# Performance work log

Hardware: AMD Instinct MI355X
Metric: run time of the kernel (lower is better)

Reference implementation:

```python
import jax, jax.numpy as jnp
import numpy as np

N = 50000
E = 800000
NUM_KINDS = 100
D_NODE = 64
D_EDGE = 4
D_MSG = 64
L = 3
D_IN = 2 * D_NODE + D_EDGE  # 132


def setup_inputs() -> dict:
    key = jax.random.key(0)
    ks = jax.random.split(key, 20)

    def w(k, shape, fan_in):
        bound = 1.0 / np.sqrt(fan_in)
        return jax.random.uniform(k, shape, jnp.float32, -bound, bound)

    inp = {
        "edge_index": jax.random.randint(ks[0], (2, E), 0, N),
        "node_kind_ids": jax.random.randint(ks[1], (N,), 0, NUM_KINDS),
        "edge_attr": jax.random.normal(ks[2], (E, D_EDGE), jnp.float32),
        # learned params
        "emb": jax.random.normal(ks[3], (NUM_KINDS, D_NODE), jnp.float32),
        # stacked per-layer message MLP params [L, ...]
        "msg_w1": w(ks[4], (L, D_MSG, D_IN), D_IN),
        "msg_b1": w(ks[5], (L, D_MSG), D_IN),
        "msg_w2": w(ks[6], (L, D_MSG, D_MSG), D_MSG),
        "msg_b2": w(ks[7], (L, D_MSG), D_MSG),
        # stacked per-layer GRUCell params (torch layout: [3*d_node, d_in])
        "gru_wih": w(ks[8], (L, 3 * D_NODE, D_MSG), D_NODE),
        "gru_whh": w(ks[9], (L, 3 * D_NODE, D_NODE), D_NODE),
        "gru_bih": w(ks[10], (L, 3 * D_NODE), D_NODE),
        "gru_bhh": w(ks[11], (L, 3 * D_NODE), D_NODE),
        # edge head: Linear(132,64) -> SiLU -> Linear(64,1)
        "head_w1": w(ks[12], (64, D_IN), D_IN),
        "head_b1": w(ks[13], (64,), D_IN),
        "head_w2": w(ks[14], (1, 64), 64),
        "head_b2": w(ks[15], (1,), 64),
    }
    return inp


def reference(edge_index, node_kind_ids, edge_attr, emb,
              msg_w1, msg_b1, msg_w2, msg_b2,
              gru_wih, gru_whh, gru_bih, gru_bhh,
              head_w1, head_b1, head_w2, head_b2):
    src, dst = edge_index[0], edge_index[1]
    h = emb[node_kind_ids]  # [N, d_node]
    n_nodes = h.shape[0]
    for l in range(L):
        x = jnp.concatenate([h[src], h[dst], edge_attr], axis=1)  # [E, 132]
        m = jax.nn.silu(x @ msg_w1[l].T + msg_b1[l]) @ msg_w2[l].T + msg_b2[l]  # [E, d_msg]
        agg = jax.ops.segment_sum(m, dst, num_segments=n_nodes)  # [N, d_msg]
        # torch GRUCell math
        gi = agg @ gru_wih[l].T + gru_bih[l]  # [N, 3*d_node]
        gh = h @ gru_whh[l].T + gru_bhh[l]
        ir, iz, inn = jnp.split(gi, 3, axis=1)
        hr, hz, hn = jnp.split(gh, 3, axis=1)
        r = jax.nn.sigmoid(ir + hr)
        z = jax.nn.sigmoid(iz + hz)
        n = jnp.tanh(inn + r * hn)
        h = (1.0 - z) * n + z * h
    x = jnp.concatenate([h[src], h[dst], edge_attr], axis=1)  # [E, 132]
    logits = (jax.nn.silu(x @ head_w1.T + head_b1) @ head_w2.T + head_b2)[:, 0]
    return jax.nn.sigmoid(logits)  # [E]
```

## Files before the change

kernel.cpp:

```cpp
#include <hip/hip_runtime.h>
#include <hip/hip_bf16.h>


typedef __attribute__((ext_vector_type(8))) short bf16x8;
typedef __attribute__((ext_vector_type(4))) float f32x4;
#define MFMA16(a, b, c) __builtin_amdgcn_mfma_f32_16x16x32_bf16(a, b, c, 0, 0, 0)

#define CHUNK 128
#define MSTRIDE 264
#define EBUF 8448
#define HIDB 4096

#define WRZST 264
#define WNST  136

__device__ __forceinline__ float fast_sig(float x) { return 1.f / (1.f + __expf(-x)); }
__device__ __forceinline__ float fast_tanh(float x) {
    float ax = fabsf(x);
    float t = __expf(-2.f * ax);
    return copysignf((1.f - t) / (1.f + t), x);
}
__device__ __forceinline__ ushort f2bf(float f) {
    unsigned u = __float_as_uint(f);
    unsigned r = u + 0x7FFF + ((u >> 16) & 1);
    return (ushort)(r >> 16);
}
__device__ __forceinline__ unsigned pkbf2(float a, float b) {
    unsigned r;
    asm("v_cvt_pk_bf16_f32 %0, %1, %2" : "=v"(r) : "v"(a), "v"(b));
    return r;
}

__global__ void prep_kernel(const float* __restrict__ msg_w1,
                            const float* __restrict__ msg_w2,
                            const float* __restrict__ gru_wih,
                            const float* __restrict__ gru_whh,
                            const float* __restrict__ head_w1,
                            const float* __restrict__ head_w2,
                            ushort* __restrict__ Wb1, ushort* __restrict__ Wb2,
                            ushort* __restrict__ Wh1, ushort* __restrict__ Wh2b,
                            ushort* __restrict__ Wrz, ushort* __restrict__ Wni,
                            ushort* __restrict__ Wnh) {
    int t = blockIdx.x * 256 + threadIdx.x;
    if (t < 30720) {
        int l = t / 10240, r = t % 10240, j = r / 160, k = r % 160;
        Wb1[t] = (k < 132) ? f2bf(msg_w1[l * 8448 + j * 132 + k]) : 0;
        return;
    }
    t -= 30720;
    if (t < 12288) {
        Wb2[t] = f2bf(msg_w2[t]);
        return;
    }
    t -= 12288;
    if (t < 10240) {
        int j = t / 160, k = t % 160;
        Wh1[t] = (k < 132) ? f2bf(head_w1[j * 132 + k]) : 0;
        return;
    }
    t -= 10240;
    if (t < 1024) {
        int j = t >> 6, k = t & 63;
        Wh2b[t] = (j == 0) ? f2bf(head_w2[k]) : 0;
        return;
    }
    t -= 1024;
    if (t < 49152) {
        int l = t / 16384, r = t % 16384, n = r >> 7, k = r & 127;
        float v = (k < 64) ? gru_wih[l * 12288 + n * 64 + k]
                           : gru_whh[l * 12288 + n * 64 + (k - 64)];
        Wrz[t] = f2bf(v);
        return;
    }
    t -= 49152;
    if (t < 12288) {
        int l = t / 4096, r = t % 4096, j = r >> 6, k = r & 63;
        Wni[t] = f2bf(gru_wih[l * 12288 + (128 + j) * 64 + k]);
        return;
    }
    t -= 12288;
    if (t < 12288) {
        int l = t / 4096, r = t % 4096, j = r >> 6, k = r & 63;
        Wnh[t] = f2bf(gru_whh[l * 12288 + (128 + j) * 64 + k]);
    }
}

__global__ void embed_kernel(float* __restrict__ h, ushort* __restrict__ hb,
                             const float* __restrict__ emb,
                             const int* __restrict__ kinds, int N) {
    int t = blockIdx.x * 256 + threadIdx.x;
    if (t >= N * 64) return;
    int node = t >> 6, d = t & 63;
    float v = emb[kinds[node] * 64 + d];
    h[t] = v;
    hb[t] = f2bf(v);
}

__global__ void hist_kernel(const int* __restrict__ dst, int* __restrict__ deg, int E) {
    int e = blockIdx.x * 256 + threadIdx.x;
    if (e < E) atomicAdd(&deg[dst[e]], 1);
}

__global__ void scan_kernel(const int* __restrict__ deg, int* __restrict__ cursor, int N) {
    __shared__ int sums[1024];
    int tid = threadIdx.x;
    int chunk = (N + 1023) >> 10;
    int lo = tid * chunk, hi = min(lo + chunk, N);
    int s = 0;
    for (int i = lo; i < hi; i++) s += deg[i];
    sums[tid] = s;
    __syncthreads();
    for (int off = 1; off < 1024; off <<= 1) {
        int v = (tid >= off) ? sums[tid - off] : 0;
        __syncthreads();
        sums[tid] += v;
        __syncthreads();
    }
    int run = (tid > 0) ? sums[tid - 1] : 0;
    for (int i = lo; i < hi; i++) {
        cursor[i] = run;
        run += deg[i];
    }
}

__global__ void scatter_kernel(const int* __restrict__ src, const int* __restrict__ dst,
                               const float* __restrict__ ea, int* __restrict__ cursor,
                               int* __restrict__ src_s, int* __restrict__ dst_s,
                               ushort* __restrict__ ea_sb, int E) {
    int e = blockIdx.x * 256 + threadIdx.x;
    if (e >= E) return;
    int d = dst[e];
    int p = atomicAdd(&cursor[d], 1);
    src_s[p] = src[e];
    dst_s[p] = d;
    float4 e4 = ((const float4*)ea)[e];
    ushort4 eb;
    eb.x = f2bf(e4.x); eb.y = f2bf(e4.y); eb.z = f2bf(e4.z); eb.w = f2bf(e4.w);
    ((ushort4*)ea_sb)[p] = eb;
}

__global__ __launch_bounds__(256) void edge_msg_mfma(
    const ushort* __restrict__ hb, const int* __restrict__ src_s,
    const int* __restrict__ dst_s, const ushort* __restrict__ ea_sb,
    const ushort* __restrict__ Wb1l, const ushort* __restrict__ Wb2l,
    const float* __restrict__ b1, const float* __restrict__ b2,
    float* __restrict__ agg, int E, int nchunks) {
    __shared__ char lds[4 * EBUF];
    int tid = threadIdx.x;
    int w = tid >> 6, lane = tid & 63;
    int quad = lane >> 4, nrow = lane & 15;
    char* buf = lds + w * EBUF;

    bf16x8 wf1[4][5];
    f32x4 b1q[4];
    float b2v[4];
#pragma unroll
    for (int nt = 0; nt < 4; nt++) {
        int n = nt * 16 + nrow;
#pragma unroll
        for (int ks = 0; ks < 5; ks++)
            wf1[nt][ks] = *(const bf16x8*)(Wb1l + n * 160 + ks * 32 + quad * 8);
        b1q[nt] = *(const f32x4*)(b1 + nt * 16 + quad * 4);
        b2v[nt] = b2[n];
    }

    for (int chunk = blockIdx.x; chunk < nchunks; chunk += gridDim.x) {
        int ebase = chunk * CHUNK + w * 32;
        int e0 = min(ebase + nrow, E - 1);
        int e1 = min(ebase + 16 + nrow, E - 1);
        int s0 = src_s[e0], s1 = src_s[e1];
        int d0 = dst_s[e0], d1 = dst_s[e1];

        bf16x8 x0[5], x1[5];
        {
            const ushort* p = hb + (size_t)s0 * 64 + quad * 8;
            x0[0] = *(const bf16x8*)p;
            x0[1] = *(const bf16x8*)(p + 32);
            p = hb + (size_t)d0 * 64 + quad * 8;
            x0[2] = *(const bf16x8*)p;
            x0[3] = *(const bf16x8*)(p + 32);
            p = hb + (size_t)s1 * 64 + quad * 8;
            x1[0] = *(const bf16x8*)p;
            x1[1] = *(const bf16x8*)(p + 32);
            p = hb + (size_t)d1 * 64 + quad * 8;
            x1[2] = *(const bf16x8*)p;
            x1[3] = *(const bf16x8*)(p + 32);
            bf16x8 z = {0, 0, 0, 0, 0, 0, 0, 0};
            x0[4] = z;
            x1[4] = z;
            if (quad == 0) {
                ushort4 v0 = *(const ushort4*)(ea_sb + (size_t)e0 * 4);
                ushort4 v1 = *(const ushort4*)(ea_sb + (size_t)e1 * 4);
                x0[4][0] = (short)v0.x; x0[4][1] = (short)v0.y;
                x0[4][2] = (short)v0.z; x0[4][3] = (short)v0.w;
                x1[4][0] = (short)v1.x; x1[4][1] = (short)v1.y;
                x1[4][2] = (short)v1.z; x1[4][3] = (short)v1.w;
            }
        }

        f32x4 acc[4][2];
#pragma unroll
        for (int nt = 0; nt < 4; nt++) {
            acc[nt][0] = b1q[nt];
            acc[nt][1] = b1q[nt];
        }
#pragma unroll
        for (int ks = 0; ks < 5; ks++)
#pragma unroll
            for (int nt = 0; nt < 4; nt++) {
                acc[nt][0] = MFMA16(wf1[nt][ks], x0[ks], acc[nt][0]);
                acc[nt][1] = MFMA16(wf1[nt][ks], x1[ks], acc[nt][1]);
            }

#pragma unroll
        for (int nt = 0; nt < 4; nt++)
#pragma unroll
            for (int et = 0; et < 2; et++) {
                f32x4 a = acc[nt][et];
                float v0 = a[0] * fast_sig(a[0]);
                float v1 = a[1] * fast_sig(a[1]);
                float v2 = a[2] * fast_sig(a[2]);
                float v3 = a[3] * fast_sig(a[3]);
                int er = et * 16 + nrow;
                int off = er * 128 + ((nt * 32 + quad * 8) ^ ((er & 7) << 4));
                uint2 pk;
                pk.x = pkbf2(v0, v1);
                pk.y = pkbf2(v2, v3);
                *(uint2*)(buf + off) = pk;
            }

        const ushort* wb2i = Wb2l;
        asm volatile("" : "+s"(wb2i));
        bf16x8 wf2[4][2];
#pragma unroll
        for (int nt = 0; nt < 4; nt++)
#pragma unroll
            for (int ks = 0; ks < 2; ks++)
                wf2[nt][ks] =
                    *(const bf16x8*)(wb2i + (nt * 16 + nrow) * 64 + ks * 32 + quad * 8);

        bf16x8 ha[2][2];
#pragma unroll
        for (int mt = 0; mt < 2; mt++)
#pragma unroll
            for (int ks = 0; ks < 2; ks++) {
                int er = mt * 16 + nrow;
                ha[mt][ks] = *(const bf16x8*)(
                    buf + er * 128 + ((ks * 64 + quad * 16) ^ ((er & 7) << 4)));
            }
        f32x4 acc2[2][4];
#pragma unroll
        for (int nt = 0; nt < 4; nt++) {
            f32x4 v;
            v[0] = v[1] = v[2] = v[3] = b2v[nt];
            acc2[0][nt] = v;
            acc2[1][nt] = v;
        }
#pragma unroll
        for (int ks = 0; ks < 2; ks++)
#pragma unroll
            for (int nt = 0; nt < 4; nt++) {
                acc2[0][nt] = MFMA16(ha[0][ks], wf2[nt][ks], acc2[0][nt]);
                acc2[1][nt] = MFMA16(ha[1][ks], wf2[nt][ks], acc2[1][nt]);
            }

#pragma unroll
        for (int mt = 0; mt < 2; mt++)
#pragma unroll
            for (int nt = 0; nt < 4; nt++)
#pragma unroll
                for (int rg = 0; rg < 4; rg++) {
                    int rm = mt * 16 + quad * 4 + rg;
                    *(float*)(buf + rm * MSTRIDE + (nt * 16 + nrow) * 4) =
                        acc2[mt][nt][rg];
                }

        {
            int dmy = (lane & 16) ? d1 : d0;
            int limit = min(32, E - ebase);
            int nx = __shfl_down(dmy, 1);
            bool tl = ((lane & 31) == 31) || (dmy != nx);
            unsigned long long tm = __ballot(tl);
            float run = 0.f;
#pragma unroll
            for (int i = 0; i < 32; i++) {
                if (i < limit) {
                    run += *(const float*)(buf + i * MSTRIDE + lane * 4);
                    if (((tm >> i) & 1ull) || (i + 1 == limit)) {
                        int di = __shfl(dmy, i);
                        unsafeAtomicAdd(&agg[(size_t)di * 64 + lane], run);
                        run = 0.f;
                    }
                }
            }
        }
    }
}

__global__ __launch_bounds__(256) void head_mfma(
    const ushort* __restrict__ hb, const int* __restrict__ src,
    const int* __restrict__ dst, const float* __restrict__ ea,
    const ushort* __restrict__ Wh1, const ushort* __restrict__ Wh2b,
    const float* __restrict__ hb1, const float* __restrict__ hb2p,
    float* __restrict__ out, int E, int nchunks) {
    __shared__ char lds[4 * HIDB];
    int tid = threadIdx.x;
    int w = tid >> 6, lane = tid & 63;
    int quad = lane >> 4, nrow = lane & 15;
    char* buf = lds + w * HIDB;

    bf16x8 wf1[4][5], wh2[2];
    f32x4 b1q[4];
#pragma unroll
    for (int nt = 0; nt < 4; nt++) {
        int n = nt * 16 + nrow;
#pragma unroll
        for (int ks = 0; ks < 5; ks++)
            wf1[nt][ks] = *(const bf16x8*)(Wh1 + n * 160 + ks * 32 + quad * 8);
        b1q[nt] = *(const f32x4*)(hb1 + nt * 16 + quad * 4);
    }
#pragma unroll
    for (int ks = 0; ks < 2; ks++)
        wh2[ks] = *(const bf16x8*)(Wh2b + nrow * 64 + ks * 32 + quad * 8);
    float hb2 = hb2p[0];

    for (int chunk = blockIdx.x; chunk < nchunks; chunk += gridDim.x) {
        int ebase = chunk * CHUNK + w * 32;
        int e0 = min(ebase + nrow, E - 1);
        int e1 = min(ebase + 16 + nrow, E - 1);
        int s0 = src[e0], s1 = src[e1];
        int d0 = dst[e0], d1 = dst[e1];

        bf16x8 x0[5], x1[5];
        {
            const ushort* p = hb + (size_t)s0 * 64 + quad * 8;
            x0[0] = *(const bf16x8*)p;
            x0[1] = *(const bf16x8*)(p + 32);
            p = hb + (size_t)d0 * 64 + quad * 8;
            x0[2] = *(const bf16x8*)p;
            x0[3] = *(const bf16x8*)(p + 32);
            p = hb + (size_t)s1 * 64 + quad * 8;
            x1[0] = *(const bf16x8*)p;
            x1[1] = *(const bf16x8*)(p + 32);
            p = hb + (size_t)d1 * 64 + quad * 8;
            x1[2] = *(const bf16x8*)p;
            x1[3] = *(const bf16x8*)(p + 32);
            bf16x8 z = {0, 0, 0, 0, 0, 0, 0, 0};
            x0[4] = z;
            x1[4] = z;
            if (quad == 0) {
                float4 q0 = ((const float4*)ea)[e0];
                float4 q1 = ((const float4*)ea)[e1];
                x0[4][0] = (short)f2bf(q0.x); x0[4][1] = (short)f2bf(q0.y);
                x0[4][2] = (short)f2bf(q0.z); x0[4][3] = (short)f2bf(q0.w);
                x1[4][0] = (short)f2bf(q1.x); x1[4][1] = (short)f2bf(q1.y);
                x1[4][2] = (short)f2bf(q1.z); x1[4][3] = (short)f2bf(q1.w);
            }
        }

        f32x4 acc[4][2];
#pragma unroll
        for (int nt = 0; nt < 4; nt++) {
            acc[nt][0] = b1q[nt];
            acc[nt][1] = b1q[nt];
        }
#pragma unroll
        for (int ks = 0; ks < 5; ks++)
#pragma unroll
            for (int nt = 0; nt < 4; nt++) {
                acc[nt][0] = MFMA16(wf1[nt][ks], x0[ks], acc[nt][0]);
                acc[nt][1] = MFMA16(wf1[nt][ks], x1[ks], acc[nt][1]);
            }

#pragma unroll
        for (int nt = 0; nt < 4; nt++)
#pragma unroll
            for (int et = 0; et < 2; et++) {
                f32x4 a = acc[nt][et];
                float v0 = a[0] * fast_sig(a[0]);
                float v1 = a[1] * fast_sig(a[1]);
                float v2 = a[2] * fast_sig(a[2]);
                float v3 = a[3] * fast_sig(a[3]);
                int er = et * 16 + nrow;
                int off = er * 128 + ((nt * 32 + quad * 8) ^ ((er & 7) << 4));
                uint2 pk;
                pk.x = pkbf2(v0, v1);
                pk.y = pkbf2(v2, v3);
                *(uint2*)(buf + off) = pk;
            }

        bf16x8 ha[2][2];
#pragma unroll
        for (int mt = 0; mt < 2; mt++)
#pragma unroll
            for (int ks = 0; ks < 2; ks++) {
                int er = mt * 16 + nrow;
                ha[mt][ks] = *(const bf16x8*)(
                    buf + er * 128 + ((ks * 64 + quad * 16) ^ ((er & 7) << 4)));
            }
        f32x4 acc3[2];
#pragma unroll
        for (int mt = 0; mt < 2; mt++) {
            f32x4 v;
            v[0] = v[1] = v[2] = v[3] = 0.f;
            acc3[mt] = v;
        }
#pragma unroll
        for (int ks = 0; ks < 2; ks++) {
            acc3[0] = MFMA16(ha[0][ks], wh2[ks], acc3[0]);
            acc3[1] = MFMA16(ha[1][ks], wh2[ks], acc3[1]);
        }
        if (nrow == 0) {
#pragma unroll
            for (int mt = 0; mt < 2; mt++)
#pragma unroll
                for (int rg = 0; rg < 4; rg++) {
                    int e = ebase + mt * 16 + quad * 4 + rg;
                    if (e < E) out[e] = fast_sig(acc3[mt][rg] + hb2);
                }
        }
    }
}

__device__ __forceinline__ bf16x8 aggfrag(const float* __restrict__ row, int off) {
    float4 f0 = *(const float4*)(row + off);
    float4 f1 = *(const float4*)(row + off + 4);
    bf16x8 r;
    r[0] = (short)f2bf(f0.x); r[1] = (short)f2bf(f0.y);
    r[2] = (short)f2bf(f0.z); r[3] = (short)f2bf(f0.w);
    r[4] = (short)f2bf(f1.x); r[5] = (short)f2bf(f1.y);
    r[6] = (short)f2bf(f1.z); r[7] = (short)f2bf(f1.w);
    return r;
}

__global__ __launch_bounds__(256) void gru_mfma(
    float* __restrict__ h, ushort* __restrict__ hb, const float* __restrict__ agg,
    const ushort* __restrict__ Wrzg, const ushort* __restrict__ Wnig,
    const ushort* __restrict__ Wnhg,
    const float* __restrict__ bih, const float* __restrict__ bhh, int N) {
    __shared__ char lds[128 * WRZST + 2 * 64 * WNST];
    int tid = threadIdx.x, w = tid >> 6, lane = tid & 63;
    int quad = lane >> 4, nrow = lane & 15;
    char* wrz = lds;
    char* wni = lds + 128 * WRZST;
    char* wnh = wni + 64 * WNST;

    {
        int r = tid >> 1, half = tid & 1;
        const uint4* g = (const uint4*)(Wrzg + r * 128 + half * 64);
        uint4* d = (uint4*)(wrz + r * WRZST + half * 128);
#pragma unroll
        for (int i = 0; i < 8; i++) d[i] = g[i];
        if (tid < 128) {
            const uint4* g2 = (const uint4*)(Wnig + (tid >> 1) * 64 + (tid & 1) * 32);
            uint4* d2 = (uint4*)(wni + (tid >> 1) * WNST + (tid & 1) * 64);
#pragma unroll
            for (int i = 0; i < 4; i++) d2[i] = g2[i];
        } else {
            int t2 = tid - 128;
            const uint4* g2 = (const uint4*)(Wnhg + (t2 >> 1) * 64 + (t2 & 1) * 32);
            uint4* d2 = (uint4*)(wnh + (t2 >> 1) * WNST + (t2 & 1) * 64);
#pragma unroll
            for (int i = 0; i < 4; i++) d2[i] = g2[i];
        }
    }
    __syncthreads();

    int nb0 = blockIdx.x * 128 + w * 32;
    if (nb0 >= N) return;

    float brz[8], bi[4], bhv[4];
#pragma unroll
    for (int nt = 0; nt < 8; nt++) brz[nt] = bih[nt * 16 + nrow] + bhh[nt * 16 + nrow];
#pragma unroll
    for (int nt = 0; nt < 4; nt++) {
        bi[nt] = bih[128 + nt * 16 + nrow];
        bhv[nt] = bhh[128 + nt * 16 + nrow];
    }

    int n0 = min(nb0 + nrow, N - 1);
    int n1 = min(nb0 + 16 + nrow, N - 1);
    const float* ag0 = agg + (size_t)n0 * 64;
    const float* ag1 = agg + (size_t)n1 * 64;
    const ushort* hb0 = hb + (size_t)n0 * 64;
    const ushort* hb1 = hb + (size_t)n1 * 64;

    f32x4 accrz[2][8], acci[2][4], acch[2][4];
#pragma unroll
    for (int nt = 0; nt < 8; nt++) {
        f32x4 v; v[0] = v[1] = v[2] = v[3] = brz[nt];
        accrz[0][nt] = v; accrz[1][nt] = v;
    }
#pragma unroll
    for (int nt = 0; nt < 4; nt++) {
        f32x4 vi; vi[0] = vi[1] = vi[2] = vi[3] = bi[nt];
        acci[0][nt] = vi; acci[1][nt] = vi;
        f32x4 vh; vh[0] = vh[1] = vh[2] = vh[3] = bhv[nt];
        acch[0][nt] = vh; acch[1][nt] = vh;
    }

#pragma unroll
    for (int ks = 0; ks < 4; ks++) {
        bf16x8 a0, a1;
        if (ks < 2) {
            a0 = aggfrag(ag0, ks * 32 + quad * 8);
            a1 = aggfrag(ag1, ks * 32 + quad * 8);
        } else {
            a0 = *(const bf16x8*)(hb0 + (ks - 2) * 32 + quad * 8);
            a1 = *(const bf16x8*)(hb1 + (ks - 2) * 32 + quad * 8);
        }
#pragma unroll
        for (int nt = 0; nt < 8; nt++) {
            bf16x8 b = *(const bf16x8*)(wrz + (nt * 16 + nrow) * WRZST + ks * 64 + quad * 16);
            accrz[0][nt] = MFMA16(a0, b, accrz[0][nt]);
            accrz[1][nt] = MFMA16(a1, b, accrz[1][nt]);
        }
        if (ks < 2) {
#pragma unroll
            for (int nt = 0; nt < 4; nt++) {
                bf16x8 b = *(const bf16x8*)(wni + (nt * 16 + nrow) * WNST + ks * 64 + quad * 16);
                acci[0][nt] = MFMA16(a0, b, acci[0][nt]);
                acci[1][nt] = MFMA16(a1, b, acci[1][nt]);
            }
        } else {
#pragma unroll
            for (int nt = 0; nt < 4; nt++) {
                bf16x8 b = *(const bf16x8*)(wnh + (nt * 16 + nrow) * WNST + (ks - 2) * 64 + quad * 16);
                acch[0][nt] = MFMA16(a0, b, acch[0][nt]);
                acch[1][nt] = MFMA16(a1, b, acch[1][nt]);
            }
        }
    }

#pragma unroll
    for (int mt = 0; mt < 2; mt++)
#pragma unroll
        for (int nt = 0; nt < 4; nt++)
#pragma unroll
            for (int rg = 0; rg < 4; rg++) {
                int node = nb0 + mt * 16 + quad * 4 + rg;
                if (node < N) {
                    int col = nt * 16 + nrow;
                    float r = fast_sig(accrz[mt][nt][rg]);
                    float z = fast_sig(accrz[mt][nt + 4][rg]);
                    float nn = fast_tanh(acci[mt][nt][rg] + r * acch[mt][nt][rg]);
                    size_t idx = (size_t)node * 64 + col;
                    float ho = h[idx];
                    float hnew = (1.f - z) * nn + z * ho;
                    h[idx] = hnew;
                    hb[idx] = f2bf(hnew);
                }
            }
}

extern "C" void kernel_launch(void* const* d_in, const int* in_sizes, int n_in,
                              void* d_out, int out_size, void* d_ws, size_t ws_size,
                              hipStream_t stream) {
    const int* edge_index = (const int*)d_in[0];
    int E = in_sizes[0] / 2;
    const int* src = edge_index;
    const int* dst = edge_index + E;
    const int* kinds = (const int*)d_in[1];
    int N = in_sizes[1];
    const float* edge_attr = (const float*)d_in[2];
    const float* emb = (const float*)d_in[3];
    const float* msg_w1 = (const float*)d_in[4];
    const float* msg_b1 = (const float*)d_in[5];
    const float* msg_w2 = (const float*)d_in[6];
    const float* msg_b2 = (const float*)d_in[7];
    const float* gru_wih = (const float*)d_in[8];
    const float* gru_whh = (const float*)d_in[9];
    const float* gru_bih = (const float*)d_in[10];
    const float* gru_bhh = (const float*)d_in[11];
    const float* head_w1 = (const float*)d_in[12];
    const float* head_b1 = (const float*)d_in[13];
    const float* head_w2 = (const float*)d_in[14];
    const float* head_b2 = (const float*)d_in[15];
    float* out = (float*)d_out;

    char* p = (char*)d_ws;
    float* h = (float*)p;        p += (size_t)N * 64 * 4;
    float* agg = (float*)p;      p += (size_t)N * 64 * 4;
    int* deg = (int*)p;          p += (size_t)N * 4;
    int* cursor = (int*)p;       p += (size_t)N * 4;
    int* src_s = (int*)p;        p += (size_t)E * 4;
    int* dst_s = (int*)p;        p += (size_t)E * 4;
    ushort* hb = (ushort*)p;     p += (size_t)N * 64 * 2;
    ushort* Wb1 = (ushort*)p;    p += 30720 * 2;
    ushort* Wb2 = (ushort*)p;    p += 12288 * 2;
    ushort* Wh1 = (ushort*)p;    p += 10240 * 2;
    ushort* Wh2b = (ushort*)p;   p += 1024 * 2;
    ushort* Wrz = (ushort*)p;    p += 49152 * 2;
    ushort* Wni = (ushort*)p;    p += 12288 * 2;
    ushort* Wnh = (ushort*)p;    p += 12288 * 2;
    ushort* ea_sb = (ushort*)p;  p += (size_t)E * 4 * 2;

    int nchunks = (E + CHUNK - 1) / CHUNK;

    prep_kernel<<<500, 256, 0, stream>>>(msg_w1, msg_w2, gru_wih, gru_whh, head_w1,
                                         head_w2, Wb1, Wb2, Wh1, Wh2b, Wrz, Wni, Wnh);
    embed_kernel<<<(N * 64 + 255) / 256, 256, 0, stream>>>(h, hb, emb, kinds, N);

    hipMemsetAsync(deg, 0, (size_t)N * sizeof(int), stream);
    hist_kernel<<<(E + 255) / 256, 256, 0, stream>>>(dst, deg, E);
    scan_kernel<<<1, 1024, 0, stream>>>(deg, cursor, N);
    scatter_kernel<<<(E + 255) / 256, 256, 0, stream>>>(src, dst, edge_attr, cursor,
                                                        src_s, dst_s, ea_sb, E);

    for (int l = 0; l < 3; l++) {
        hipMemsetAsync(agg, 0, (size_t)N * 64 * sizeof(float), stream);
        edge_msg_mfma<<<1024, 256, 0, stream>>>(
            hb, src_s, dst_s, ea_sb,
            Wb1 + l * 10240, Wb2 + l * 4096,
            msg_b1 + l * 64, msg_b2 + l * 64, agg, E, nchunks);
        gru_mfma<<<(N + 127) / 128, 256, 0, stream>>>(
            h, hb, agg, Wrz + l * 16384, Wni + l * 4096, Wnh + l * 4096,
            gru_bih + l * 192, gru_bhh + l * 192, N);
    }
    head_mfma<<<1024, 256, 0, stream>>>(hb, src, dst, edge_attr, Wh1, Wh2b,
                                        head_b1, head_b2, out, E, nchunks);
}
```

Before: 699.6 us.

## Fold layer-1 biases into padded weight columns and cap register use for occupancy

Folds the first-layer bias of the message MLP and the edge head into the zero-padded K columns of the bf16 weight matrices, using a hi/lo bf16 split of each bias, with constant-one inputs in the matching activation slots. This removes the per-lane bias registers, and accumulator arrays are reused across the two GEMM stages. Together with __launch_bounds__(256,3) and a reduced grid of 768 blocks, the aim is to cut VGPR pressure so three blocks fit per CU. The risk is spilling under the tighter register cap and slight bias precision change from the split representation.

```diff
diff --git a/kernel.cpp b/kernel.cpp
--- a/kernel.cpp
+++ b/kernel.cpp
@@ -25,6 +25,9 @@
     unsigned r = u + 0x7FFF + ((u >> 16) & 1);
     return (ushort)(r >> 16);
 }
+__device__ __forceinline__ float bf2f(ushort b) {
+    return __uint_as_float(((unsigned)b) << 16);
+}
 __device__ __forceinline__ unsigned pkbf2(float a, float b) {
     unsigned r;
     asm("v_cvt_pk_bf16_f32 %0, %1, %2" : "=v"(r) : "v"(a), "v"(b));
@@ -32,10 +35,12 @@
 }
 
 __global__ void prep_kernel(const float* __restrict__ msg_w1,
+                            const float* __restrict__ msg_b1,
                             const float* __restrict__ msg_w2,
                             const float* __restrict__ gru_wih,
                             const float* __restrict__ gru_whh,
                             const float* __restrict__ head_w1,
+                            const float* __restrict__ head_b1,
                             const float* __restrict__ head_w2,
                             ushort* __restrict__ Wb1, ushort* __restrict__ Wb2,
                             ushort* __restrict__ Wh1, ushort* __restrict__ Wh2b,
@@ -44,7 +49,16 @@
     int t = blockIdx.x * 256 + threadIdx.x;
     if (t < 30720) {
         int l = t / 10240, r = t % 10240, j = r / 160, k = r % 160;
-        Wb1[t] = (k < 132) ? f2bf(msg_w1[l * 8448 + j * 132 + k]) : 0;
+        float v = 0.f;
+        if (k < 132) {
+            v = msg_w1[l * 8448 + j * 132 + k];
+        } else if (k == 132) {
+            v = msg_b1[l * 64 + j];
+        } else if (k == 133) {
+            float b = msg_b1[l * 64 + j];
+            v = b - bf2f(f2bf(b));
+        }
+        Wb1[t] = f2bf(v);
         return;
     }
     t -= 30720;
@@ -55,7 +69,16 @@
     t -= 12288;
     if (t < 10240) {
         int j = t / 160, k = t % 160;
-        Wh1[t] = (k < 132) ? f2bf(head_w1[j * 132 + k]) : 0;
+        float v = 0.f;
+        if (k < 132) {
+            v = head_w1[j * 132 + k];
+        } else if (k == 132) {
+            v = head_b1[j];
+        } else if (k == 133) {
+            float b = head_b1[j];
+            v = b - bf2f(f2bf(b));
+        }
+        Wh1[t] = f2bf(v);
         return;
     }
     t -= 10240;
@@ -139,11 +162,11 @@
     ((ushort4*)ea_sb)[p] = eb;
 }
 
-__global__ __launch_bounds__(256) void edge_msg_mfma(
+__global__ __launch_bounds__(256, 3) void edge_msg_mfma(
     const ushort* __restrict__ hb, const int* __restrict__ src_s,
     const int* __restrict__ dst_s, const ushort* __restrict__ ea_sb,
     const ushort* __restrict__ Wb1l, const ushort* __restrict__ Wb2l,
-    const float* __restrict__ b1, const float* __restrict__ b2,
+    const float* __restrict__ b2,
     float* __restrict__ agg, int E, int nchunks) {
     __shared__ char lds[4 * EBUF];
     int tid = threadIdx.x;
@@ -152,7 +175,6 @@
     char* buf = lds + w * EBUF;
 
     bf16x8 wf1[4][5];
-    f32x4 b1q[4];
     float b2v[4];
 #pragma unroll
     for (int nt = 0; nt < 4; nt++) {
@@ -160,7 +182,6 @@
 #pragma unroll
         for (int ks = 0; ks < 5; ks++)
             wf1[nt][ks] = *(const bf16x8*)(Wb1l + n * 160 + ks * 32 + quad * 8);
-        b1q[nt] = *(const f32x4*)(b1 + nt * 16 + quad * 4);
         b2v[nt] = b2[n];
     }
 
@@ -193,30 +214,33 @@
                 ushort4 v1 = *(const ushort4*)(ea_sb + (size_t)e1 * 4);
                 x0[4][0] = (short)v0.x; x0[4][1] = (short)v0.y;
                 x0[4][2] = (short)v0.z; x0[4][3] = (short)v0.w;
+                x0[4][4] = (short)0x3F80; x0[4][5] = (short)0x3F80;
                 x1[4][0] = (short)v1.x; x1[4][1] = (short)v1.y;
                 x1[4][2] = (short)v1.z; x1[4][3] = (short)v1.w;
-            }
-        }
-
-        f32x4 acc[4][2];
-#pragma unroll
-        for (int nt = 0; nt < 4; nt++) {
-            acc[nt][0] = b1q[nt];
-            acc[nt][1] = b1q[nt];
+                x1[4][4] = (short)0x3F80; x1[4][5] = (short)0x3F80;
+            }
+        }
+
+        f32x4 acc[8];
+        {
+            f32x4 z4;
+            z4[0] = z4[1] = z4[2] = z4[3] = 0.f;
+#pragma unroll
+            for (int i = 0; i < 8; i++) acc[i] = z4;
         }
 #pragma unroll
         for (int ks = 0; ks < 5; ks++)
 #pragma unroll
             for (int nt = 0; nt < 4; nt++) {
-                acc[nt][0] = MFMA16(wf1[nt][ks], x0[ks], acc[nt][0]);
-                acc[nt][1] = MFMA16(wf1[nt][ks], x1[ks], acc[nt][1]);
+                acc[nt * 2 + 0] = MFMA16(wf1[nt][ks], x0[ks], acc[nt * 2 + 0]);
+                acc[nt * 2 + 1] = MFMA16(wf1[nt][ks], x1[ks], acc[nt * 2 + 1]);
             }
 
 #pragma unroll
         for (int nt = 0; nt < 4; nt++)
 #pragma unroll
             for (int et = 0; et < 2; et++) {
-                f32x4 a = acc[nt][et];
+                f32x4 a = acc[nt * 2 + et];
                 float v0 = a[0] * fast_sig(a[0]);
                 float v1 = a[1] * fast_sig(a[1]);
                 float v2 = a[2] * fast_sig(a[2]);
@@ -248,20 +272,20 @@
                 ha[mt][ks] = *(const bf16x8*)(
                     buf + er * 128 + ((ks * 64 + quad * 16) ^ ((er & 7) << 4)));
             }
-        f32x4 acc2[2][4];
-#pragma unroll
-        for (int nt = 0; nt < 4; nt++) {
-            f32x4 v;
-            v[0] = v[1] = v[2] = v[3] = b2v[nt];
-            acc2[0][nt] = v;
-            acc2[1][nt] = v;
-        }
+#pragma unroll
+        for (int mt = 0; mt < 2; mt++)
+#pragma unroll
+            for (int nt = 0; nt < 4; nt++) {
+                f32x4 v;
+                v[0] = v[1] = v[2] = v[3] = b2v[nt];
+                acc[mt * 4 + nt] = v;
+            }
 #pragma unroll
         for (int ks = 0; ks < 2; ks++)
 #pragma unroll
             for (int nt = 0; nt < 4; nt++) {
-                acc2[0][nt] = MFMA16(ha[0][ks], wf2[nt][ks], acc2[0][nt]);
-                acc2[1][nt] = MFMA16(ha[1][ks], wf2[nt][ks], acc2[1][nt]);
+                acc[0 * 4 + nt] = MFMA16(ha[0][ks], wf2[nt][ks], acc[0 * 4 + nt]);
+                acc[1 * 4 + nt] = MFMA16(ha[1][ks], wf2[nt][ks], acc[1 * 4 + nt]);
             }
 
 #pragma unroll
@@ -272,7 +296,7 @@
                 for (int rg = 0; rg < 4; rg++) {
                     int rm = mt * 16 + quad * 4 + rg;
                     *(float*)(buf + rm * MSTRIDE + (nt * 16 + nrow) * 4) =
-                        acc2[mt][nt][rg];
+                        acc[mt * 4 + nt][rg];
                 }
 
         {
@@ -297,11 +321,11 @@
     }
 }
 
-__global__ __launch_bounds__(256) void head_mfma(
+__global__ __launch_bounds__(256, 3) void head_mfma(
     const ushort* __restrict__ hb, const int* __restrict__ src,
     const int* __restrict__ dst, const float* __restrict__ ea,
     const ushort* __restrict__ Wh1, const ushort* __restrict__ Wh2b,
-    const float* __restrict__ hb1, const float* __restrict__ hb2p,
+    const float* __restrict__ hb2p,
     float* __restrict__ out, int E, int nchunks) {
     __shared__ char lds[4 * HIDB];
     int tid = threadIdx.x;
@@ -309,19 +333,14 @@
     int quad = lane >> 4, nrow = lane & 15;
     char* buf = lds + w * HIDB;
 
-    bf16x8 wf1[4][5], wh2[2];
-    f32x4 b1q[4];
+    bf16x8 wf1[4][5];
 #pragma unroll
     for (int nt = 0; nt < 4; nt++) {
         int n = nt * 16 + nrow;
 #pragma unroll
         for (int ks = 0; ks < 5; ks++)
             wf1[nt][ks] = *(const bf16x8*)(Wh1 + n * 160 + ks * 32 + quad * 8);
-        b1q[nt] = *(const f32x4*)(hb1 + nt * 16 + quad * 4);
-    }
-#pragma unroll
-    for (int ks = 0; ks < 2; ks++)
-        wh2[ks] = *(const bf16x8*)(Wh2b + nrow * 64 + ks * 32 + quad * 8);
+    }
     float hb2 = hb2p[0];
 
     for (int chunk = blockIdx.x; chunk < nchunks; chunk += gridDim.x) {
@@ -353,30 +372,33 @@
                 float4 q1 = ((const float4*)ea)[e1];
                 x0[4][0] = (short)f2bf(q0.x); x0[4][1] = (short)f2bf(q0.y);
                 x0[4][2] = (short)f2bf(q0.z); x0[4][3] = (short)f2bf(q0.w);
+                x0[4][4] = (short)0x3F80; x0[4][5] = (short)0x3F80;
                 x1[4][0] = (short)f2bf(q1.x); x1[4][1] = (short)f2bf(q1.y);
                 x1[4][2] = (short)f2bf(q1.z); x1[4][3] = (short)f2bf(q1.w);
-            }
-        }
-
-        f32x4 acc[4][2];
-#pragma unroll
-        for (int nt = 0; nt < 4; nt++) {
-            acc[nt][0] = b1q[nt];
-            acc[nt][1] = b1q[nt];
+                x1[4][4] = (short)0x3F80; x1[4][5] = (short)0x3F80;
+            }
+        }
+
+        f32x4 acc[8];
+        {
+            f32x4 z4;
+            z4[0] = z4[1] = z4[2] = z4[3] = 0.f;
+#pragma unroll
+            for (int i = 0; i < 8; i++) acc[i] = z4;
         }
 #pragma unroll
         for (int ks = 0; ks < 5; ks++)
 #pragma unroll
             for (int nt = 0; nt < 4; nt++) {
-                acc[nt][0] = MFMA16(wf1[nt][ks], x0[ks], acc[nt][0]);
-                acc[nt][1] = MFMA16(wf1[nt][ks], x1[ks], acc[nt][1]);
+                acc[nt * 2 + 0] = MFMA16(wf1[nt][ks], x0[ks], acc[nt * 2 + 0]);
+                acc[nt * 2 + 1] = MFMA16(wf1[nt][ks], x1[ks], acc[nt * 2 + 1]);
             }
 
 #pragma unroll
         for (int nt = 0; nt < 4; nt++)
 #pragma unroll
             for (int et = 0; et < 2; et++) {
-                f32x4 a = acc[nt][et];
+                f32x4 a = acc[nt * 2 + et];
                 float v0 = a[0] * fast_sig(a[0]);
                 float v1 = a[1] * fast_sig(a[1]);
                 float v2 = a[2] * fast_sig(a[2]);
@@ -389,6 +411,13 @@
                 *(uint2*)(buf + off) = pk;
             }
 
+        const ushort* wh2i = Wh2b;
+        asm volatile("" : "+s"(wh2i));
+        bf16x8 wh2[2];
+#pragma unroll
+        for (int ks = 0; ks < 2; ks++)
+            wh2[ks] = *(const bf16x8*)(wh2i + nrow * 64 + ks * 32 + quad * 8);
+
         bf16x8 ha[2][2];
 #pragma unroll
         for (int mt = 0; mt < 2; mt++)
@@ -398,17 +427,16 @@
                 ha[mt][ks] = *(const bf16x8*)(
                     buf + er * 128 + ((ks * 64 + quad * 16) ^ ((er & 7) << 4)));
             }
-        f32x4 acc3[2];
-#pragma unroll
-        for (int mt = 0; mt < 2; mt++) {
-            f32x4 v;
-            v[0] = v[1] = v[2] = v[3] = 0.f;
-            acc3[mt] = v;
+        {
+            f32x4 z4;
+            z4[0] = z4[1] = z4[2] = z4[3] = 0.f;
+            acc[0] = z4;
+            acc[1] = z4;
         }
 #pragma unroll
         for (int ks = 0; ks < 2; ks++) {
-            acc3[0] = MFMA16(ha[0][ks], wh2[ks], acc3[0]);
-            acc3[1] = MFMA16(ha[1][ks], wh2[ks], acc3[1]);
+            acc[0] = MFMA16(ha[0][ks], wh2[ks], acc[0]);
+            acc[1] = MFMA16(ha[1][ks], wh2[ks], acc[1]);
         }
         if (nrow == 0) {
 #pragma unroll
@@ -416,7 +444,7 @@
 #pragma unroll
                 for (int rg = 0; rg < 4; rg++) {
                     int e = ebase + mt * 16 + quad * 4 + rg;
-                    if (e < E) out[e] = fast_sig(acc3[mt][rg] + hb2);
+                    if (e < E) out[e] = fast_sig(acc[mt][rg] + hb2);
                 }
         }
     }
@@ -597,8 +625,9 @@
 
     int nchunks = (E + CHUNK - 1) / CHUNK;
 
-    prep_kernel<<<500, 256, 0, stream>>>(msg_w1, msg_w2, gru_wih, gru_whh, head_w1,
-                                         head_w2, Wb1, Wb2, Wh1, Wh2b, Wrz, Wni, Wnh);
+    prep_kernel<<<500, 256, 0, stream>>>(msg_w1, msg_b1, msg_w2, gru_wih, gru_whh,
+                                         head_w1, head_b1, head_w2,
+                                         Wb1, Wb2, Wh1, Wh2b, Wrz, Wni, Wnh);
     embed_kernel<<<(N * 64 + 255) / 256, 256, 0, stream>>>(h, hb, emb, kinds, N);
 
     hipMemsetAsync(deg, 0, (size_t)N * sizeof(int), stream);
@@ -609,14 +638,14 @@
 
     for (int l = 0; l < 3; l++) {
         hipMemsetAsync(agg, 0, (size_t)N * 64 * sizeof(float), stream);
-        edge_msg_mfma<<<1024, 256, 0, stream>>>(
+        edge_msg_mfma<<<768, 256, 0, stream>>>(
             hb, src_s, dst_s, ea_sb,
             Wb1 + l * 10240, Wb2 + l * 4096,
-            msg_b1 + l * 64, msg_b2 + l * 64, agg, E, nchunks);
+            msg_b2 + l * 64, agg, E, nchunks);
         gru_mfma<<<(N + 127) / 128, 256, 0, stream>>>(
             h, hb, agg, Wrz + l * 16384, Wni + l * 4096, Wnh + l * 4096,
             gru_bih + l * 192, gru_bhh + l * 192, N);
     }
-    head_mfma<<<1024, 256, 0, stream>>>(hb, src, dst, edge_attr, Wh1, Wh2b,
-                                        head_b1, head_b2, out, E, nchunks);
-}
+    head_mfma<<<768, 256, 0, stream>>>(hb, src, dst, edge_attr, Wh1, Wh2b,
+                                       head_b2, out, E, nchunks);
+}
```

Result: faster. 673.8 us (-3.7%).
